# Kernel optimization log

Hardware: AMD Instinct MI355X
Metric: run time of the kernel (lower is better)

## Reference

```python
import jax, jax.numpy as jnp
import numpy as np

HIDDEN = 1024
NUM_HEADS = 16
HEAD_DIM = HIDDEN // NUM_HEADS
ROPE_THETA = 10000.0


def rope_tables(seq_len, head_dim, theta):
    inv_freq = 1.0 / theta ** (jnp.arange(0, head_dim, 2, dtype=jnp.float32) / head_dim)
    pos = jnp.arange(seq_len, dtype=jnp.float32)
    freqs = jnp.outer(pos, inv_freq)  # [S, hd/2]
    return jnp.cos(freqs), jnp.sin(freqs)


def apply_rope(x, cos, sin):
    # x: [B, nh, S, hd]; cos/sin: [S, hd/2]
    x1, x2 = jnp.split(x, 2, axis=-1)
    return jnp.concatenate([x1 * cos - x2 * sin, x2 * cos + x1 * sin], axis=-1)


def setup_inputs() -> dict:
    key = jax.random.key(0)
    k1, k2, k3 = jax.random.split(key, 3)
    B, S = 2, 2048
    hidden_states = jax.random.normal(k1, (B, S, HIDDEN), dtype=jnp.float32)
    # nn.Linear stores weight as [out, in]; y = x @ W.T
    Wqkv = jax.random.normal(k2, (3 * HIDDEN, HIDDEN), dtype=jnp.float32) * (HIDDEN ** -0.5)
    Wo = jax.random.normal(k3, (HIDDEN, HIDDEN), dtype=jnp.float32) * (HIDDEN ** -0.5)
    return {"hidden_states": hidden_states, "Wqkv": Wqkv, "Wo": Wo}


def reference(hidden_states, Wqkv, Wo):
    B, S, H = hidden_states.shape
    qkv = hidden_states @ Wqkv.T  # [B, S, 3H]
    qkv = qkv.reshape(B, S, 3, NUM_HEADS, HEAD_DIM)
    q, k, v = jnp.moveaxis(qkv, 2, 0)  # each [B, S, nh, hd]
    q = jnp.transpose(q, (0, 2, 1, 3))  # [B, nh, S, hd]
    k = jnp.transpose(k, (0, 2, 1, 3))
    v = jnp.transpose(v, (0, 2, 1, 3))
    cos, sin = rope_tables(S, HEAD_DIM, ROPE_THETA)
    q = apply_rope(q, cos, sin)
    k = apply_rope(k, cos, sin)
    scale = 1.0 / jnp.sqrt(jnp.asarray(HEAD_DIM, dtype=q.dtype))
    scores = jnp.einsum("bhqd,bhkd->bhqk", q, k) * scale
    causal = jnp.tril(jnp.ones((S, S), dtype=bool))
    scores = jnp.where(causal, scores, jnp.finfo(scores.dtype).min)
    attn = jax.nn.softmax(scores, axis=-1)
    out = jnp.einsum("bhqk,bhkd->bhqd", attn, v)  # [B, nh, S, hd]
    out = jnp.transpose(out, (0, 2, 1, 3)).reshape(B, S, H)
    return out @ Wo.T
```

## Files before the change

### kernel.cpp

```cpp
#include <hip/hip_runtime.h>
#include <hip/hip_bf16.h>
#include <math.h>

typedef __bf16 bf16_t;
typedef __attribute__((ext_vector_type(8))) __bf16 bf16x8;
typedef __attribute__((ext_vector_type(4))) float f32x4;
typedef __attribute__((ext_vector_type(16))) float f32x16;
typedef __attribute__((ext_vector_type(4))) unsigned u32x4;

#define AS1(p) ((__attribute__((address_space(1))) void*)(p))
#define AS3(p) ((__attribute__((address_space(3))) void*)(p))

__device__ inline void cvt8(const float* __restrict__ in, bf16_t* __restrict__ out, int i) {
  const float4* p = (const float4*)in;
  float4 a = p[2 * i], b = p[2 * i + 1];
  bf16x8 o;
  o[0] = (bf16_t)a.x; o[1] = (bf16_t)a.y; o[2] = (bf16_t)a.z; o[3] = (bf16_t)a.w;
  o[4] = (bf16_t)b.x; o[5] = (bf16_t)b.y; o[6] = (bf16_t)b.z; o[7] = (bf16_t)b.w;
  ((bf16x8*)out)[i] = o;
}

__global__ __launch_bounds__(256)
void prep_all(const float* __restrict__ hid, const float* __restrict__ wqkv,
              const float* __restrict__ wo, bf16_t* __restrict__ hidb,
              bf16_t* __restrict__ wqkvb, bf16_t* __restrict__ wob,
              float* __restrict__ cosb, float* __restrict__ sinb) {
  const int bid = blockIdx.x, tid = threadIdx.x;
  if (bid < 2048) {
    cvt8(hid, hidb, bid * 256 + tid);
  } else if (bid < 3584) {
    cvt8(wqkv, wqkvb, (bid - 2048) * 256 + tid);
  } else if (bid < 4096) {
    cvt8(wo, wob, (bid - 3584) * 256 + tid);
  } else {
    int t = (bid - 4096) * 256 + tid;
    int s = t >> 5, i = t & 31;
    float inv = powf(10000.0f, -(float)i / 32.0f);
    float sv, cv;
    sincosf((float)s * inv, &sv, &cv);
    cosb[t] = cv;
    sinb[t] = sv;
  }
}

__global__ __launch_bounds__(256)
void pack_rope(bf16_t* __restrict__ qkv, const float* __restrict__ cosb,
               const float* __restrict__ sinb, bf16_t* __restrict__ Kp) {
  __shared__ bf16_t vl[64][72];
  const int t = blockIdx.x, bh = blockIdx.y, b = bh >> 4, h = bh & 15;
  const int tid = threadIdx.x;
  const int r = tid >> 2, j = tid & 3;
  const int s = t * 64 + r;
  bf16_t* base = qkv + ((size_t)(b * 2048 + s)) * 3072 + h * 64;
  const float* cb = cosb + s * 32 + j * 8;
  const float* sb = sinb + s * 32 + j * 8;
  bf16x8 q1 = *(const bf16x8*)(base + j * 8);
  bf16x8 q2 = *(const bf16x8*)(base + j * 8 + 32);
  bf16x8 k1 = *(const bf16x8*)(base + 1024 + j * 8);
  bf16x8 k2 = *(const bf16x8*)(base + 1024 + j * 8 + 32);
  bf16x8 v1 = *(const bf16x8*)(base + 2048 + j * 8);
  bf16x8 v2 = *(const bf16x8*)(base + 2048 + j * 8 + 32);
  const float QS = 0.125f * 1.4426950408889634f;
  bf16x8 qo1, qo2, ko1, ko2;
#pragma unroll
  for (int i = 0; i < 8; ++i) {
    float c = cb[i], sn = sb[i];
    float a1 = (float)q1[i], a2 = (float)q2[i];
    qo1[i] = (bf16_t)((a1 * c - a2 * sn) * QS);
    qo2[i] = (bf16_t)((a2 * c + a1 * sn) * QS);
    float b1 = (float)k1[i], b2 = (float)k2[i];
    ko1[i] = (bf16_t)(b1 * c - b2 * sn);
    ko2[i] = (bf16_t)(b2 * c + b1 * sn);
  }
  *(bf16x8*)(base + j * 8) = qo1;
  *(bf16x8*)(base + j * 8 + 32) = qo2;
  bf16_t* kd = Kp + ((size_t)(bh * 32 + t)) * 4096 + r * 64;
  *(bf16x8*)(kd + ((j ^ (r & 7)) * 8)) = ko1;
  *(bf16x8*)(kd + (((j + 4) ^ (r & 7)) * 8)) = ko2;
#pragma unroll
  for (int i = 0; i < 8; ++i) { vl[r][j * 8 + i] = v1[i]; vl[r][j * 8 + 32 + i] = v2[i]; }
  __syncthreads();
  const int d = r;
  bf16x8 o1, o2;
#pragma unroll
  for (int i = 0; i < 8; ++i) { o1[i] = vl[j * 16 + i][d]; o2[i] = vl[j * 16 + 8 + i][d]; }
  bf16_t* vd = base + 2048;
  *(bf16x8*)(vd + (((2 * j) ^ (d & 7)) * 8)) = o1;
  *(bf16x8*)(vd + (((2 * j + 1) ^ (d & 7)) * 8)) = o2;
}

template <typename OutT>
__global__ __launch_bounds__(256, 2)
void gemm_nt(const bf16_t* __restrict__ A, const bf16_t* __restrict__ B,
             OutT* __restrict__ C, int M, int N, int K) {
  __shared__ __align__(16) bf16_t lA[128 * 64];
  __shared__ __align__(16) bf16_t lB[128 * 64];
  const int tid = threadIdx.x;
  const int wid = tid >> 6, lane = tid & 63;
  const int lr = lane & 15, lg = lane >> 4;
  const int nwg = gridDim.x * gridDim.y;
  int lin = blockIdx.y * gridDim.x + blockIdx.x;
  lin = (lin & 7) * (nwg >> 3) + (lin >> 3);
  const int m0 = (lin / gridDim.x) * 128, n0 = (lin % gridDim.x) * 128;
  const int wm = (wid >> 1) * 64, wn = (wid & 1) * 64;
  const int srow = lane >> 3;
  const int scol = (lane & 7) * 8;
  f32x4 acc[4][4];
#pragma unroll
  for (int i = 0; i < 4; ++i)
#pragma unroll
    for (int j = 0; j < 4; ++j) acc[i][j] = f32x4{0.f, 0.f, 0.f, 0.f};

  const int nk = K >> 6;
  for (int kt = 0; kt < nk; ++kt) {
    const int k0 = kt << 6;
    __syncthreads();
#pragma unroll
    for (int i = 0; i < 4; ++i) {
      int c = (wid << 2) + i;
      int r = (c << 3) + srow;
      __builtin_amdgcn_global_load_lds(AS1(A + (size_t)(m0 + r) * K + k0 + scol),
                                       AS3(&lA[c * 512]), 16, 0, 0);
      __builtin_amdgcn_global_load_lds(AS1(B + (size_t)(n0 + r) * K + k0 + scol),
                                       AS3(&lB[c * 512]), 16, 0, 0);
    }
    __syncthreads();
#pragma unroll
    for (int ks = 0; ks < 2; ++ks) {
      bf16x8 af[4], bfr[4];
#pragma unroll
      for (int i = 0; i < 4; ++i) {
        af[i]  = *(const bf16x8*)&lA[(wm + i * 16 + lr) * 64 + ks * 32 + lg * 8];
        bfr[i] = *(const bf16x8*)&lB[(wn + i * 16 + lr) * 64 + ks * 32 + lg * 8];
      }
#pragma unroll
      for (int i = 0; i < 4; ++i)
#pragma unroll
        for (int j = 0; j < 4; ++j)
          acc[i][j] = __builtin_amdgcn_mfma_f32_16x16x32_bf16(af[i], bfr[j], acc[i][j], 0, 0, 0);
    }
  }
#pragma unroll
  for (int i = 0; i < 4; ++i)
#pragma unroll
    for (int j = 0; j < 4; ++j)
#pragma unroll
      for (int r = 0; r < 4; ++r) {
        int row = m0 + wm + i * 16 + lg * 4 + r;
        int col = n0 + wn + j * 16 + lr;
        C[(size_t)row * N + col] = (OutT)acc[i][j][r];
      }
}

__device__ inline unsigned pkbf(float a, float b) {
  bf16_t x = (bf16_t)a, y = (bf16_t)b;
  return (unsigned)__builtin_bit_cast(unsigned short, x) |
         ((unsigned)__builtin_bit_cast(unsigned short, y) << 16);
}
__device__ inline f32x16 zero16() {
  f32x16 z;
#pragma unroll
  for (int r = 0; r < 16; ++r) z[r] = 0.f;
  return z;
}

__global__ __launch_bounds__(128, 2)
void attn_fwd(const bf16_t* __restrict__ qkv, const bf16_t* __restrict__ Kp,
              bf16_t* __restrict__ O) {
  __shared__ __align__(16) bf16_t Ksh[2][4096];
  __shared__ __align__(16) bf16_t Vsh[2][4096];
  const int tid = threadIdx.x, wid = tid >> 6, lane = tid & 63;
  const int ln = lane & 31, h = lane >> 5;
  const int lin = blockIdx.x;
  const int g = lin >> 8, j = lin & 255;
  const int bh = j & 31, cc = j >> 5;
  const int c = (g == 0) ? 31 - cc : (g == 1) ? 16 + cc : (g == 2) ? 15 - cc : cc;
  const int b = bh >> 4, hd = bh & 15;
  const int NI = c + 1;
  const int qw = c * 64 + wid * 32;

  const bf16_t* Qrow = qkv + ((size_t)(b * 2048 + qw + ln)) * 3072 + hd * 64;
  bf16x8 qf[4];
#pragma unroll
  for (int t = 0; t < 4; ++t) qf[t] = *(const bf16x8*)(Qrow + t * 16 + h * 8);

  f32x16 o0 = zero16(), o1 = zero16();
  float lp = 0.f;

  const bf16_t* Kbase = Kp + ((size_t)bh * 32) * 4096 + tid * 8;
  const bf16_t* Vbase = qkv + ((size_t)(b * 2048 + (tid >> 3))) * 3072 + 2048 + hd * 64 + (tid & 7) * 8;

#define STAGE(T, BUF)                                                                     \
  do {                                                                                    \
    const bf16_t* ks = Kbase + (size_t)(T) * 4096;                                        \
    __builtin_amdgcn_global_load_lds(AS1(ks),        AS3(&Ksh[BUF][tid * 8]), 16, 0, 0);  \
    __builtin_amdgcn_global_load_lds(AS1(ks + 1024), AS3(&Ksh[BUF][1024 + tid * 8]), 16, 0, 0); \
    __builtin_amdgcn_global_load_lds(AS1(ks + 2048), AS3(&Ksh[BUF][2048 + tid * 8]), 16, 0, 0); \
    __builtin_amdgcn_global_load_lds(AS1(ks + 3072), AS3(&Ksh[BUF][3072 + tid * 8]), 16, 0, 0); \
    const bf16_t* vs = Vbase + (size_t)(T) * 64 * 3072;                                   \
    __builtin_amdgcn_global_load_lds(AS1(vs),             AS3(&Vsh[BUF][tid * 8]), 16, 0, 0);        \
    __builtin_amdgcn_global_load_lds(AS1(vs + 16 * 3072), AS3(&Vsh[BUF][1024 + tid * 8]), 16, 0, 0); \
    __builtin_amdgcn_global_load_lds(AS1(vs + 32 * 3072), AS3(&Vsh[BUF][2048 + tid * 8]), 16, 0, 0); \
    __builtin_amdgcn_global_load_lds(AS1(vs + 48 * 3072), AS3(&Vsh[BUF][3072 + tid * 8]), 16, 0, 0); \
  } while (0)

  STAGE(0, 0);
  for (int i = 0; i < NI; ++i) {
    asm volatile("s_waitcnt vmcnt(0)" ::: "memory");
    __builtin_amdgcn_s_barrier();
    if (i + 1 < NI) STAGE(i + 1, (i + 1) & 1);
    const bf16_t* K = &Ksh[i & 1][0];
    const bf16_t* V = &Vsh[i & 1][0];
    f32x16 s0 = zero16(), s1 = zero16();
    __builtin_amdgcn_s_setprio(1);
#pragma unroll
    for (int t = 0; t < 4; ++t) {
      const int ch = 2 * t + h;
      bf16x8 k0 = *(const bf16x8*)&K[ln * 64 + ((ch ^ (ln & 7)) * 8)];
      bf16x8 k1 = *(const bf16x8*)&K[(32 + ln) * 64 + ((ch ^ (ln & 7)) * 8)];
      s0 = __builtin_amdgcn_mfma_f32_32x32x16_bf16(k0, qf[t], s0, 0, 0, 0);
      s1 = __builtin_amdgcn_mfma_f32_32x32x16_bf16(k1, qf[t], s1, 0, 0, 0);
    }
    __builtin_amdgcn_s_setprio(0);
    if (i == NI - 1) {
      const int qg = qw + ln, k0g = i * 64;
#pragma unroll
      for (int r = 0; r < 16; ++r) {
        int kv = k0g + (r & 3) + 8 * (r >> 2) + 4 * h;
        if (kv > qg) s0[r] = -3e38f;
        if (kv + 32 > qg) s1[r] = -3e38f;
      }
    }
#pragma unroll
    for (int r = 0; r < 16; ++r) {
      float p0 = __builtin_amdgcn_exp2f(s0[r]); lp += p0; s0[r] = p0;
      float p1 = __builtin_amdgcn_exp2f(s1[r]); lp += p1; s1[r] = p1;
    }
    __builtin_amdgcn_s_setprio(1);
#pragma unroll
    for (int t = 0; t < 4; ++t) {
      const int u = t & 1;
      f32x16 sv = (t >> 1) ? s1 : s0;
      unsigned x  = pkbf(sv[8 * u + 0], sv[8 * u + 1]);
      unsigned x2 = pkbf(sv[8 * u + 2], sv[8 * u + 3]);
      unsigned y  = pkbf(sv[8 * u + 4], sv[8 * u + 5]);
      unsigned y2 = pkbf(sv[8 * u + 6], sv[8 * u + 7]);
      asm volatile("v_permlane32_swap_b32 %0, %1" : "+v"(x), "+v"(y));
      asm volatile("v_permlane32_swap_b32 %0, %1" : "+v"(x2), "+v"(y2));
      u32x4 pw; pw[0] = x; pw[1] = x2; pw[2] = y; pw[3] = y2;
      bf16x8 pf = __builtin_bit_cast(bf16x8, pw);
      const int ch = 2 * t + h;
      bf16x8 v0 = *(const bf16x8*)&V[ln * 64 + ((ch ^ (ln & 7)) * 8)];
      bf16x8 v1 = *(const bf16x8*)&V[(32 + ln) * 64 + ((ch ^ (ln & 7)) * 8)];
      o0 = __builtin_amdgcn_mfma_f32_32x32x16_bf16(v0, pf, o0, 0, 0, 0);
      o1 = __builtin_amdgcn_mfma_f32_32x32x16_bf16(v1, pf, o1, 0, 0, 0);
    }
    __builtin_amdgcn_s_setprio(0);
  }
#undef STAGE
  {
    float lpf = lp + __shfl_xor(lp, 32, 64);
    float inv = 1.0f / lpf;
    bf16_t* Oaddr = O + ((size_t)(b * 2048 + qw + ln)) * 1024 + hd * 64;
#pragma unroll
    for (int D = 0; D < 2; ++D) {
      f32x16 ov = D ? o1 : o0;
#pragma unroll
      for (int Q = 0; Q < 4; ++Q) {
        uint2 w;
        w.x = pkbf(ov[4 * Q + 0] * inv, ov[4 * Q + 1] * inv);
        w.y = pkbf(ov[4 * Q + 2] * inv, ov[4 * Q + 3] * inv);
        *(uint2*)(Oaddr + D * 32 + Q * 8 + 4 * h) = w;
      }
    }
  }
}

extern "C" void kernel_launch(void* const* d_in, const int* in_sizes, int n_in,
                              void* d_out, int out_size, void* d_ws, size_t ws_size,
                              hipStream_t stream) {
  const float* hid  = (const float*)d_in[0];
  const float* wqkv = (const float*)d_in[1];
  const float* wo   = (const float*)d_in[2];
  float* out = (float*)d_out;
  char* ws = (char*)d_ws;
  bf16_t* hidb  = (bf16_t*)(ws);
  bf16_t* wqkvb = (bf16_t*)(ws + 8388608);
  bf16_t* wob   = (bf16_t*)(ws + 14680064);
  bf16_t* qkvb  = (bf16_t*)(ws + 16777216);
  float*  cosb  = (float*)(ws + 41943040);
  float*  sinb  = (float*)(ws + 42205184);
  bf16_t* Ob    = (bf16_t*)(ws + 42467328);
  bf16_t* Kp    = (bf16_t*)(ws);

  prep_all<<<4352, 256, 0, stream>>>(hid, wqkv, wo, hidb, wqkvb, wob, cosb, sinb);
  gemm_nt<bf16_t><<<dim3(24, 32), 256, 0, stream>>>(hidb, wqkvb, qkvb, 4096, 3072, 1024);
  pack_rope<<<dim3(32, 32), 256, 0, stream>>>(qkvb, cosb, sinb, Kp);
  attn_fwd<<<1024, 128, 0, stream>>>(qkvb, Kp, Ob);
  gemm_nt<float><<<dim3(8, 32), 256, 0, stream>>>(Ob, wob, out, 4096, 1024, 1024);
}
```

Measured before the change: 122.0 us.

## Split long causal attention chunks across two KV halves and combine partials

Query chunks 20–31 are split into two work items, each covering half of the KV tiles. A lookup table orders the 1408 blocks so the heaviest items are scheduled first. Each half writes unnormalized bf16 partial outputs and row sums to reused workspace, and a new combine kernel adds them and normalizes. This targets tail imbalance from the long causal rows, at the cost of an extra launch, partial-result traffic and bf16 rounding of the intermediate sums.

```diff
diff --git a/kernel.cpp b/kernel.cpp
--- a/kernel.cpp
+++ b/kernel.cpp
@@ -164,19 +164,31 @@
   return z;
 }
 
+__device__ const unsigned char ROLE_LUT[44] = {
+    19, 18, 17, 16,
+    15, 95, 159, 158,
+    14, 94, 93, 157,
+    13, 92, 156, 91, 155, 154,
+    12, 90, 89, 153, 152,
+    11, 88, 87, 151, 150,
+    10, 86, 85, 149, 148,
+    9, 84,
+    8, 7, 6, 5, 4, 3, 2, 1, 0};
+
 __global__ __launch_bounds__(128, 2)
 void attn_fwd(const bf16_t* __restrict__ qkv, const bf16_t* __restrict__ Kp,
-              bf16_t* __restrict__ O) {
+              bf16_t* __restrict__ O, bf16_t* __restrict__ Po, float* __restrict__ Plp) {
   __shared__ __align__(16) bf16_t Ksh[2][4096];
   __shared__ __align__(16) bf16_t Vsh[2][4096];
   const int tid = threadIdx.x, wid = tid >> 6, lane = tid & 63;
   const int ln = lane & 31, h = lane >> 5;
   const int lin = blockIdx.x;
-  const int g = lin >> 8, j = lin & 255;
-  const int bh = j & 31, cc = j >> 5;
-  const int c = (g == 0) ? 31 - cc : (g == 1) ? 16 + cc : (g == 2) ? 15 - cc : cc;
+  const int e = ROLE_LUT[lin >> 5];
+  const int bh = lin & 31;
+  const int c = e & 31, kind = e >> 6;
   const int b = bh >> 4, hd = bh & 15;
-  const int NI = c + 1;
+  const int t0 = (kind == 2) ? ((c + 1) >> 1) : 0;
+  const int t1 = (kind == 1) ? ((c + 1) >> 1) : c + 1;
   const int qw = c * 64 + wid * 32;
 
   const bf16_t* Qrow = qkv + ((size_t)(b * 2048 + qw + ln)) * 3072 + hd * 64;
@@ -204,26 +216,26 @@
     __builtin_amdgcn_global_load_lds(AS1(vs + 48 * 3072), AS3(&Vsh[BUF][3072 + tid * 8]), 16, 0, 0); \
   } while (0)
 
-  STAGE(0, 0);
-  for (int i = 0; i < NI; ++i) {
+  STAGE(t0, t0 & 1);
+  for (int t = t0; t < t1; ++t) {
     asm volatile("s_waitcnt vmcnt(0)" ::: "memory");
     __builtin_amdgcn_s_barrier();
-    if (i + 1 < NI) STAGE(i + 1, (i + 1) & 1);
-    const bf16_t* K = &Ksh[i & 1][0];
-    const bf16_t* V = &Vsh[i & 1][0];
+    if (t + 1 < t1) STAGE(t + 1, (t + 1) & 1);
+    const bf16_t* K = &Ksh[t & 1][0];
+    const bf16_t* V = &Vsh[t & 1][0];
     f32x16 s0 = zero16(), s1 = zero16();
     __builtin_amdgcn_s_setprio(1);
 #pragma unroll
-    for (int t = 0; t < 4; ++t) {
-      const int ch = 2 * t + h;
+    for (int u = 0; u < 4; ++u) {
+      const int ch = 2 * u + h;
       bf16x8 k0 = *(const bf16x8*)&K[ln * 64 + ((ch ^ (ln & 7)) * 8)];
       bf16x8 k1 = *(const bf16x8*)&K[(32 + ln) * 64 + ((ch ^ (ln & 7)) * 8)];
-      s0 = __builtin_amdgcn_mfma_f32_32x32x16_bf16(k0, qf[t], s0, 0, 0, 0);
-      s1 = __builtin_amdgcn_mfma_f32_32x32x16_bf16(k1, qf[t], s1, 0, 0, 0);
+      s0 = __builtin_amdgcn_mfma_f32_32x32x16_bf16(k0, qf[u], s0, 0, 0, 0);
+      s1 = __builtin_amdgcn_mfma_f32_32x32x16_bf16(k1, qf[u], s1, 0, 0, 0);
     }
     __builtin_amdgcn_s_setprio(0);
-    if (i == NI - 1) {
-      const int qg = qw + ln, k0g = i * 64;
+    if (t == c) {
+      const int qg = qw + ln, k0g = t * 64;
 #pragma unroll
       for (int r = 0; r < 16; ++r) {
         int kv = k0g + (r & 3) + 8 * (r >> 2) + 4 * h;
@@ -238,18 +250,18 @@
     }
     __builtin_amdgcn_s_setprio(1);
 #pragma unroll
-    for (int t = 0; t < 4; ++t) {
-      const int u = t & 1;
-      f32x16 sv = (t >> 1) ? s1 : s0;
-      unsigned x  = pkbf(sv[8 * u + 0], sv[8 * u + 1]);
-      unsigned x2 = pkbf(sv[8 * u + 2], sv[8 * u + 3]);
-      unsigned y  = pkbf(sv[8 * u + 4], sv[8 * u + 5]);
-      unsigned y2 = pkbf(sv[8 * u + 6], sv[8 * u + 7]);
+    for (int u = 0; u < 4; ++u) {
+      const int w = u & 1;
+      f32x16 sv = (u >> 1) ? s1 : s0;
+      unsigned x  = pkbf(sv[8 * w + 0], sv[8 * w + 1]);
+      unsigned x2 = pkbf(sv[8 * w + 2], sv[8 * w + 3]);
+      unsigned y  = pkbf(sv[8 * w + 4], sv[8 * w + 5]);
+      unsigned y2 = pkbf(sv[8 * w + 6], sv[8 * w + 7]);
       asm volatile("v_permlane32_swap_b32 %0, %1" : "+v"(x), "+v"(y));
       asm volatile("v_permlane32_swap_b32 %0, %1" : "+v"(x2), "+v"(y2));
       u32x4 pw; pw[0] = x; pw[1] = x2; pw[2] = y; pw[3] = y2;
       bf16x8 pf = __builtin_bit_cast(bf16x8, pw);
-      const int ch = 2 * t + h;
+      const int ch = 2 * u + h;
       bf16x8 v0 = *(const bf16x8*)&V[ln * 64 + ((ch ^ (ln & 7)) * 8)];
       bf16x8 v1 = *(const bf16x8*)&V[(32 + ln) * 64 + ((ch ^ (ln & 7)) * 8)];
       o0 = __builtin_amdgcn_mfma_f32_32x32x16_bf16(v0, pf, o0, 0, 0, 0);
@@ -258,8 +270,8 @@
     __builtin_amdgcn_s_setprio(0);
   }
 #undef STAGE
-  {
-    float lpf = lp + __shfl_xor(lp, 32, 64);
+  float lpf = lp + __shfl_xor(lp, 32, 64);
+  if (kind == 0) {
     float inv = 1.0f / lpf;
     bf16_t* Oaddr = O + ((size_t)(b * 2048 + qw + ln)) * 1024 + hd * 64;
 #pragma unroll
@@ -273,6 +285,45 @@
         *(uint2*)(Oaddr + D * 32 + Q * 8 + 4 * h) = w;
       }
     }
+  } else {
+    const int slot = (bh * 12 + (c - 20)) * 2 + (kind - 1);
+    const int qi = wid * 32 + ln;
+    if (h == 0) Plp[slot * 64 + qi] = lpf;
+    bf16_t* Paddr = Po + ((size_t)(slot * 64 + qi)) * 64;
+#pragma unroll
+    for (int D = 0; D < 2; ++D) {
+      f32x16 ov = D ? o1 : o0;
+#pragma unroll
+      for (int Q = 0; Q < 4; ++Q) {
+        uint2 w;
+        w.x = pkbf(ov[4 * Q + 0], ov[4 * Q + 1]);
+        w.y = pkbf(ov[4 * Q + 2], ov[4 * Q + 3]);
+        *(uint2*)(Paddr + D * 32 + Q * 8 + 4 * h) = w;
+      }
+    }
+  }
+}
+
+__global__ __launch_bounds__(64)
+void attn_combine(const bf16_t* __restrict__ Po, const float* __restrict__ Plp,
+                  bf16_t* __restrict__ O) {
+  const int blk = blockIdx.x;
+  const int bh = blk / 12, sc = blk % 12;
+  const int b = bh >> 4, hd = bh & 15;
+  const int c = 20 + sc;
+  const int q = threadIdx.x;
+  const int slotA = (bh * 12 + sc) * 2, slotB = slotA + 1;
+  float inv = 1.0f / (Plp[slotA * 64 + q] + Plp[slotB * 64 + q]);
+  const bf16x8* pa = (const bf16x8*)(Po + ((size_t)(slotA * 64 + q)) * 64);
+  const bf16x8* pb = (const bf16x8*)(Po + ((size_t)(slotB * 64 + q)) * 64);
+  bf16_t* oaddr = O + ((size_t)(b * 2048 + c * 64 + q)) * 1024 + hd * 64;
+#pragma unroll
+  for (int j = 0; j < 8; ++j) {
+    bf16x8 a = pa[j], v = pb[j];
+    bf16x8 w;
+#pragma unroll
+    for (int k = 0; k < 8; ++k) w[k] = (bf16_t)(((float)a[k] + (float)v[k]) * inv);
+    ((bf16x8*)oaddr)[j] = w;
   }
 }
 
@@ -292,10 +343,13 @@
   float*  sinb  = (float*)(ws + 42205184);
   bf16_t* Ob    = (bf16_t*)(ws + 42467328);
   bf16_t* Kp    = (bf16_t*)(ws);
+  bf16_t* Po    = (bf16_t*)(ws + 8388608);
+  float*  Plp   = (float*)(ws + 41943040);
 
   prep_all<<<4352, 256, 0, stream>>>(hid, wqkv, wo, hidb, wqkvb, wob, cosb, sinb);
   gemm_nt<bf16_t><<<dim3(24, 32), 256, 0, stream>>>(hidb, wqkvb, qkvb, 4096, 3072, 1024);
   pack_rope<<<dim3(32, 32), 256, 0, stream>>>(qkvb, cosb, sinb, Kp);
-  attn_fwd<<<1024, 128, 0, stream>>>(qkvb, Kp, Ob);
+  attn_fwd<<<1408, 128, 0, stream>>>(qkvb, Kp, Ob, Po, Plp);
+  attn_combine<<<384, 64, 0, stream>>>(Po, Plp, Ob);
   gemm_nt<float><<<dim3(8, 32), 256, 0, stream>>>(Ob, wob, out, 4096, 1024, 1024);
 }
```

After: 118.9 us. -2.5%, faster.
